# Optimization experiments

Measured on AMD Instinct MI355X. Metric: run time of the kernel, lower is better.

## Reference

```python
import jax, jax.numpy as jnp
from jax import lax
import numpy as np

FDIM = 32          # feature channels
FSIZE = 128        # 2**base_lod, grid has FSIZE+1 points per axis
G = FSIZE + 1
HID = 128          # decoder hidden dim
DOMAIN = 1.2       # FeatureVolume.domain_range
N_PTS = 1_048_576

# 8 corner offsets in (dz, dy, dx) order
_CORNERS = np.array([[0,0,0],[0,0,1],[0,1,0],[0,1,1],
                     [1,0,0],[1,0,1],[1,1,0],[1,1,1]], dtype=np.int32)


def setup_inputs() -> dict:
    key = jax.random.key(0)
    k1, k2, k3, k4, k5, k6 = jax.random.split(key, 6)
    x = jax.random.uniform(k1, (N_PTS, 3), jnp.float32, -DOMAIN, DOMAIN)
    fm = jax.random.normal(k2, (FDIM, G, G, G), jnp.float32) * 0.01
    din = FDIM + 3  # pos_invariant=False -> concat(x, features)
    W1 = jax.random.normal(k3, (HID, din), jnp.float32) * (1.0 / np.sqrt(din))
    b1 = jnp.zeros((HID,), jnp.float32)
    W2 = jax.random.normal(k4, (1, HID), jnp.float32) * (1.0 / np.sqrt(HID))
    b2 = jnp.zeros((1,), jnp.float32)
    return {"x": x, "fm": fm, "W1": W1, "b1": b1, "W2": W2, "b2": b2}


def _trilinear_sample(fm, coords):
    """Faithful jax port of grid_sample_3d (align_corners=True, border clamp).
    fm: [C, ID, IH, IW], coords: [N, 3] in (x, y, z) normalized to [-1, 1].
    Returns [N, C].
    """
    C, ID, IH, IW = fm.shape
    ix = (coords[:, 0] + 1.0) * 0.5 * (IW - 1)
    iy = (coords[:, 1] + 1.0) * 0.5 * (IH - 1)
    iz = (coords[:, 2] + 1.0) * 0.5 * (ID - 1)
    # floors are computed under no_grad in the original
    ix0 = lax.stop_gradient(jnp.floor(ix))
    iy0 = lax.stop_gradient(jnp.floor(iy))
    iz0 = lax.stop_gradient(jnp.floor(iz))
    fx, fy, fz = ix - ix0, iy - iy0, iz - iz0  # fractional offsets, [N]
    wx = jnp.stack([1.0 - fx, fx])  # [2, N]
    wy = jnp.stack([1.0 - fy, fy])
    wz = jnp.stack([1.0 - fz, fz])
    off = jnp.asarray(_CORNERS)  # [8, 3] (dz, dy, dx)
    # per-corner trilinear weights [8, N] (same products as tnw..bse)
    w = wz[off[:, 0]] * wy[off[:, 1]] * wx[off[:, 2]]
    # clamped integer corner indices [8, N]
    xi = jnp.clip(ix0[None] + off[:, 2, None], 0, IW - 1).astype(jnp.int32)
    yi = jnp.clip(iy0[None] + off[:, 1, None], 0, IH - 1).astype(jnp.int32)
    zi = jnp.clip(iz0[None] + off[:, 0, None], 0, ID - 1).astype(jnp.int32)
    flat = (zi * IH + yi) * IW + xi  # [8, N]
    vals = fm.reshape(C, -1)[:, flat]  # [C, 8, N] gather
    return jnp.einsum('ckn,kn->nc', vals, w)


def reference(x, fm, W1, b1, W2, b2):
    # FeatureVolume: normalize by domain_range then trilinear-sample the grid
    feat = _trilinear_sample(fm, x / DOMAIN)          # [N, FDIM]
    ex = jnp.concatenate([x, feat], axis=-1)          # [N, 3 + FDIM]
    h = jax.nn.relu(ex @ W1.T + b1)                   # [N, HID]
    d = h @ W2.T + b2                                 # [N, 1]
    return d.reshape(1, -1, 1)                        # return_dict['pred']
```

## Files before the change

kernel.cpp:

```cpp
#include <hip/hip_runtime.h>
#include <hip/hip_bf16.h>

#define GQ 129
#define S_TOTAL (129*129*129)
#define FDIM 32
#define HID 128
#define DIN 35
#define ROWP 40

__device__ __forceinline__ float bf_lo(unsigned u) { return __uint_as_float(u << 16); }
__device__ __forceinline__ float bf_hi(unsigned u) { return __uint_as_float(u & 0xffff0000u); }

__global__ __launch_bounds__(256) void transpose_vol(const float* __restrict__ fm,
                                                     unsigned* __restrict__ vol)
{
    int s = blockIdx.x * 256 + threadIdx.x;
    if (s >= S_TOTAL) return;
    unsigned pk[16];
#pragma unroll
    for (int j = 0; j < 16; ++j) {
        float a = fm[(size_t)(2*j)     * S_TOTAL + s];
        float b = fm[(size_t)(2*j + 1) * S_TOTAL + s];
        unsigned ua = __float_as_uint(a); ua = (ua + 0x7fffu + ((ua >> 16) & 1u)) >> 16;
        unsigned ub = __float_as_uint(b); ub = (ub + 0x7fffu + ((ub >> 16) & 1u)) >> 16;
        pk[j] = ua | (ub << 16);
    }
    uint4* o = (uint4*)(vol + (size_t)s * 16);
#pragma unroll
    for (int j = 0; j < 4; ++j)
        o[j] = make_uint4(pk[4*j], pk[4*j+1], pk[4*j+2], pk[4*j+3]);
}

__device__ __forceinline__ float mlp_eval(const float* __restrict__ sW1,
                                          const float* __restrict__ sb1,
                                          const float* __restrict__ sW2,
                                          float sb2v,
                                          float px, float py, float pz,
                                          const float feat[FDIM])
{
    float accum = sb2v;
#pragma unroll 4
    for (int h = 0; h < HID; ++h) {
        const float* wr = sW1 + h * ROWP;
        float a = sb1[h];
        a = fmaf(wr[0], px, a);
        a = fmaf(wr[1], py, a);
        a = fmaf(wr[2], pz, a);
        const float4* wf = (const float4*)(wr + 4);
#pragma unroll
        for (int j = 0; j < 8; ++j) {
            float4 w4 = wf[j];
            a = fmaf(w4.x, feat[4*j+0], a);
            a = fmaf(w4.y, feat[4*j+1], a);
            a = fmaf(w4.z, feat[4*j+2], a);
            a = fmaf(w4.w, feat[4*j+3], a);
        }
        accum = fmaf(sW2[h], fmaxf(a, 0.0f), accum);
    }
    return accum;
}

__device__ __forceinline__ void stage_weights(const float* __restrict__ W1,
                                              const float* __restrict__ b1,
                                              const float* __restrict__ W2,
                                              const float* __restrict__ b2,
                                              float* sW1, float* sb1, float* sW2,
                                              float* sb2v)
{
    int t = threadIdx.x;
    for (int i = t; i < HID * DIN; i += 256) {
        int h = i / DIN, c = i % DIN;
        sW1[h * ROWP + (c < 3 ? c : c + 1)] = W1[i];
    }
    if (t < HID) { sb1[t] = b1[t]; sW2[t] = W2[t]; }
    if (t == 0)  { *sb2v = b2[0]; }
    __syncthreads();
}

__global__ __launch_bounds__(256) void sample_mlp(const float* __restrict__ x,
                                                  const unsigned* __restrict__ vol,
                                                  const float* __restrict__ W1,
                                                  const float* __restrict__ b1,
                                                  const float* __restrict__ W2,
                                                  const float* __restrict__ b2,
                                                  float* __restrict__ out, int npts)
{
    __shared__ float sW1[HID * ROWP];
    __shared__ float sb1[HID];
    __shared__ float sW2[HID];
    __shared__ float sb2v;
    stage_weights(W1, b1, W2, b2, sW1, sb1, sW2, &sb2v);

    int p = blockIdx.x * 256 + threadIdx.x;
    if (p >= npts) return;

    float px = x[3*p + 0], py = x[3*p + 1], pz = x[3*p + 2];
    const float SC = 64.0f / 1.2f;
    float ix = fmaf(px, SC, 64.0f);
    float iy = fmaf(py, SC, 64.0f);
    float iz = fmaf(pz, SC, 64.0f);
    float fx0 = floorf(ix), fy0 = floorf(iy), fz0 = floorf(iz);
    float fx = ix - fx0, fy = iy - fy0, fz = iz - fz0;
    int ix0 = (int)fx0, iy0 = (int)fy0, iz0 = (int)fz0;
    int x0 = min(max(ix0, 0), GQ-1), x1 = min(max(ix0 + 1, 0), GQ-1);
    int y0 = min(max(iy0, 0), GQ-1), y1 = min(max(iy0 + 1, 0), GQ-1);
    int z0 = min(max(iz0, 0), GQ-1), z1 = min(max(iz0 + 1, 0), GQ-1);

    float feat[FDIM];
#pragma unroll
    for (int c = 0; c < FDIM; ++c) feat[c] = 0.0f;

#pragma unroll
    for (int k = 0; k < 8; ++k) {
        int zi = (k & 4) ? z1 : z0;
        int yi = (k & 2) ? y1 : y0;
        int xi = (k & 1) ? x1 : x0;
        float w = ((k & 4) ? fz : 1.0f - fz)
                * ((k & 2) ? fy : 1.0f - fy)
                * ((k & 1) ? fx : 1.0f - fx);
        const uint4* q = (const uint4*)(vol + (size_t)((zi * GQ + yi) * GQ + xi) * 16);
#pragma unroll
        for (int j = 0; j < 4; ++j) {
            uint4 v = q[j];
            feat[8*j + 0] = fmaf(w, bf_lo(v.x), feat[8*j + 0]);
            feat[8*j + 1] = fmaf(w, bf_hi(v.x), feat[8*j + 1]);
            feat[8*j + 2] = fmaf(w, bf_lo(v.y), feat[8*j + 2]);
            feat[8*j + 3] = fmaf(w, bf_hi(v.y), feat[8*j + 3]);
            feat[8*j + 4] = fmaf(w, bf_lo(v.z), feat[8*j + 4]);
            feat[8*j + 5] = fmaf(w, bf_hi(v.z), feat[8*j + 5]);
            feat[8*j + 6] = fmaf(w, bf_lo(v.w), feat[8*j + 6]);
            feat[8*j + 7] = fmaf(w, bf_hi(v.w), feat[8*j + 7]);
        }
    }

    out[p] = mlp_eval(sW1, sb1, sW2, sb2v, px, py, pz, feat);
}

__global__ __launch_bounds__(256) void sample_mlp_direct(const float* __restrict__ x,
                                                         const float* __restrict__ fm,
                                                         const float* __restrict__ W1,
                                                         const float* __restrict__ b1,
                                                         const float* __restrict__ W2,
                                                         const float* __restrict__ b2,
                                                         float* __restrict__ out, int npts)
{
    __shared__ float sW1[HID * ROWP];
    __shared__ float sb1[HID];
    __shared__ float sW2[HID];
    __shared__ float sb2v;
    stage_weights(W1, b1, W2, b2, sW1, sb1, sW2, &sb2v);

    int p = blockIdx.x * 256 + threadIdx.x;
    if (p >= npts) return;

    float px = x[3*p + 0], py = x[3*p + 1], pz = x[3*p + 2];
    const float SC = 64.0f / 1.2f;
    float ix = fmaf(px, SC, 64.0f);
    float iy = fmaf(py, SC, 64.0f);
    float iz = fmaf(pz, SC, 64.0f);
    float fx0 = floorf(ix), fy0 = floorf(iy), fz0 = floorf(iz);
    float fx = ix - fx0, fy = iy - fy0, fz = iz - fz0;
    int ix0 = (int)fx0, iy0 = (int)fy0, iz0 = (int)fz0;
    int x0 = min(max(ix0, 0), GQ-1), x1 = min(max(ix0 + 1, 0), GQ-1);
    int y0 = min(max(iy0, 0), GQ-1), y1 = min(max(iy0 + 1, 0), GQ-1);
    int z0 = min(max(iz0, 0), GQ-1), z1 = min(max(iz0 + 1, 0), GQ-1);

    int  sidx[8];
    float cw[8];
#pragma unroll
    for (int k = 0; k < 8; ++k) {
        int zi = (k & 4) ? z1 : z0;
        int yi = (k & 2) ? y1 : y0;
        int xi = (k & 1) ? x1 : x0;
        sidx[k] = (zi * GQ + yi) * GQ + xi;
        cw[k] = ((k & 4) ? fz : 1.0f - fz)
              * ((k & 2) ? fy : 1.0f - fy)
              * ((k & 1) ? fx : 1.0f - fx);
    }

    float feat[FDIM];
#pragma unroll
    for (int c = 0; c < FDIM; ++c) {
        const float* base = fm + (size_t)c * S_TOTAL;
        float a = 0.0f;
#pragma unroll
        for (int k = 0; k < 8; ++k) a = fmaf(cw[k], base[sidx[k]], a);
        feat[c] = a;
    }

    out[p] = mlp_eval(sW1, sb1, sW2, sb2v, px, py, pz, feat);
}

extern "C" void kernel_launch(void* const* d_in, const int* in_sizes, int n_in,
                              void* d_out, int out_size, void* d_ws, size_t ws_size,
                              hipStream_t stream)
{
    const float* x  = (const float*)d_in[0];
    const float* fm = (const float*)d_in[1];
    const float* W1 = (const float*)d_in[2];
    const float* b1 = (const float*)d_in[3];
    const float* W2 = (const float*)d_in[4];
    const float* b2 = (const float*)d_in[5];
    float* out = (float*)d_out;
    int npts = in_sizes[0] / 3;

    size_t need = (size_t)S_TOTAL * FDIM * sizeof(unsigned short);
    if (ws_size >= need) {
        unsigned* vol = (unsigned*)d_ws;
        transpose_vol<<<(S_TOTAL + 255) / 256, 256, 0, stream>>>(fm, vol);
        sample_mlp<<<(npts + 255) / 256, 256, 0, stream>>>(x, vol, W1, b1, W2, b2, out, npts);
    } else {
        sample_mlp_direct<<<(npts + 255) / 256, 256, 0, stream>>>(x, fm, W1, b1, W2, b2, out, npts);
    }
}
```

Measured before the change: 581.8 us.

## Replace scalar MLP with bf16 MFMA over 16-point tiles per wave

Replaces the per-thread scalar FMA decoder with a wave-level bf16 MFMA path. Each wave processes 16 points per tile, with 4 lane groups each gathering an 8-channel slice of the corner features. Positions and their first-layer weights use a hi/lo bf16 split to keep precision. The kernel runs as a grid-stride loop of 512 blocks, keeps the weights in registers instead of LDS, and reduces the second layer with cross-lane shuffles. The trade-off is extra bf16 rounding of the sampled features and an x-load pattern with limited coalescing.

```diff
diff --git a/kernel.cpp b/kernel.cpp
--- a/kernel.cpp
+++ b/kernel.cpp
@@ -8,8 +8,18 @@
 #define DIN 35
 #define ROWP 40
 
+typedef short short8 __attribute__((ext_vector_type(8)));
+typedef float f32x4  __attribute__((ext_vector_type(4)));
+
 __device__ __forceinline__ float bf_lo(unsigned u) { return __uint_as_float(u << 16); }
 __device__ __forceinline__ float bf_hi(unsigned u) { return __uint_as_float(u & 0xffff0000u); }
+__device__ __forceinline__ unsigned short f2bf(float f) {
+    unsigned u = __float_as_uint(f);
+    return (unsigned short)((u + 0x7fffu + ((u >> 16) & 1u)) >> 16);
+}
+__device__ __forceinline__ float bf2f(unsigned short h) {
+    return __uint_as_float(((unsigned)h) << 16);
+}
 
 __global__ __launch_bounds__(256) void transpose_vol(const float* __restrict__ fm,
                                                      unsigned* __restrict__ vol)
@@ -29,6 +39,147 @@
 #pragma unroll
     for (int j = 0; j < 4; ++j)
         o[j] = make_uint4(pk[4*j], pk[4*j+1], pk[4*j+2], pk[4*j+3]);
+}
+
+__global__ __launch_bounds__(256) void sample_mlp_mfma(const float* __restrict__ x,
+                                                       const unsigned* __restrict__ vol,
+                                                       const float* __restrict__ W1,
+                                                       const float* __restrict__ b1,
+                                                       const float* __restrict__ W2,
+                                                       const float* __restrict__ b2,
+                                                       float* __restrict__ out, int npts)
+{
+    const int lane = threadIdx.x & 63;
+    const int wave = blockIdx.x * 4 + (threadIdx.x >> 6);
+    const int nwaves = gridDim.x * 4;
+    const int c = lane & 15;
+    const int g = lane >> 4;
+
+    short8 B0[8], B1[8];
+    float b1v[8], w2v[8];
+#pragma unroll
+    for (int t = 0; t < 8; ++t) {
+        const float* wr = W1 + (t*16 + c) * DIN;
+        short8 f0 = (short8)0, f1 = (short8)0;
+        if (g == 0) {
+            short h0 = (short)f2bf(wr[0]), h1 = (short)f2bf(wr[1]), h2 = (short)f2bf(wr[2]);
+            f0[0] = h0; f0[1] = h1; f0[2] = h2; f0[3] = h0; f0[4] = h1; f0[5] = h2;
+#pragma unroll
+            for (int j = 0; j < 8; ++j) f1[j] = (short)f2bf(wr[3 + 16 + j]);
+        } else if (g == 1) {
+#pragma unroll
+            for (int d = 0; d < 3; ++d) {
+                unsigned short hh = f2bf(wr[d]);
+                f0[d] = (short)f2bf(wr[d] - bf2f(hh));
+            }
+#pragma unroll
+            for (int j = 0; j < 8; ++j) f1[j] = (short)f2bf(wr[3 + 24 + j]);
+        } else if (g == 2) {
+#pragma unroll
+            for (int j = 0; j < 8; ++j) f0[j] = (short)f2bf(wr[3 + j]);
+        } else {
+#pragma unroll
+            for (int j = 0; j < 8; ++j) f0[j] = (short)f2bf(wr[3 + 8 + j]);
+        }
+        B0[t] = f0; B1[t] = f1;
+        b1v[t] = b1[t*16 + c];
+        w2v[t] = W2[t*16 + c];
+    }
+    const float b2v = b2[0];
+
+    const int cb = ((g + 2) & 3) * 8;
+    const char* volb = (const char*)vol + cb * 2;
+
+    const int ntiles = (npts + 15) >> 4;
+    for (int tile = wave; tile < ntiles; tile += nwaves) {
+        const int p0 = tile << 4;
+        const int p  = p0 + c;
+        const int pc = min(p, npts - 1);
+        float px = x[3*pc], py = x[3*pc + 1], pz = x[3*pc + 2];
+        const float SC = 64.0f / 1.2f;
+        float ix = fmaf(px, SC, 64.0f), iy = fmaf(py, SC, 64.0f), iz = fmaf(pz, SC, 64.0f);
+        float fx0 = floorf(ix), fy0 = floorf(iy), fz0 = floorf(iz);
+        float fx = ix - fx0, fy = iy - fy0, fz = iz - fz0;
+        int ix0 = (int)fx0, iy0 = (int)fy0, iz0 = (int)fz0;
+        int x0 = min(max(ix0, 0), GQ-1), x1 = min(max(ix0 + 1, 0), GQ-1);
+        int y0 = min(max(iy0, 0), GQ-1), y1 = min(max(iy0 + 1, 0), GQ-1);
+        int z0 = min(max(iz0, 0), GQ-1), z1 = min(max(iz0 + 1, 0), GQ-1);
+
+        uint4 cv[8]; float w8[8];
+#pragma unroll
+        for (int k = 0; k < 8; ++k) {
+            int zi = (k & 4) ? z1 : z0;
+            int yi = (k & 2) ? y1 : y0;
+            int xi = (k & 1) ? x1 : x0;
+            w8[k] = ((k & 4) ? fz : 1.0f - fz)
+                  * ((k & 2) ? fy : 1.0f - fy)
+                  * ((k & 1) ? fx : 1.0f - fx);
+            cv[k] = *(const uint4*)(volb + (size_t)((zi*GQ + yi)*GQ + xi) * 64);
+        }
+        float F[8];
+#pragma unroll
+        for (int j = 0; j < 8; ++j) F[j] = 0.0f;
+#pragma unroll
+        for (int k = 0; k < 8; ++k) {
+            float w = w8[k]; uint4 v = cv[k];
+            F[0] = fmaf(w, bf_lo(v.x), F[0]); F[1] = fmaf(w, bf_hi(v.x), F[1]);
+            F[2] = fmaf(w, bf_lo(v.y), F[2]); F[3] = fmaf(w, bf_hi(v.y), F[3]);
+            F[4] = fmaf(w, bf_lo(v.z), F[4]); F[5] = fmaf(w, bf_hi(v.z), F[5]);
+            F[6] = fmaf(w, bf_lo(v.w), F[6]); F[7] = fmaf(w, bf_hi(v.w), F[7]);
+        }
+        short8 Fp;
+#pragma unroll
+        for (int j = 0; j < 8; ++j) Fp[j] = (short)f2bf(F[j]);
+
+        short8 A0, A1;
+        if (g < 2) {
+            unsigned short xh0 = f2bf(px), xh1 = f2bf(py), xh2 = f2bf(pz);
+            A0 = (short8)0;
+            A0[0] = (short)xh0; A0[1] = (short)xh1; A0[2] = (short)xh2;
+            if (g == 0) {
+                A0[3] = (short)f2bf(px - bf2f(xh0));
+                A0[4] = (short)f2bf(py - bf2f(xh1));
+                A0[5] = (short)f2bf(pz - bf2f(xh2));
+            }
+            A1 = Fp;
+        } else {
+            A0 = Fp;
+            A1 = (short8)0;
+        }
+
+        f32x4 acc[8];
+#pragma unroll
+        for (int t = 0; t < 8; ++t) { f32x4 z = {0.f, 0.f, 0.f, 0.f}; acc[t] = z; }
+#pragma unroll
+        for (int t = 0; t < 8; ++t) {
+            acc[t] = __builtin_amdgcn_mfma_f32_16x16x32_bf16(A0, B0[t], acc[t], 0, 0, 0);
+            acc[t] = __builtin_amdgcn_mfma_f32_16x16x32_bf16(A1, B1[t], acc[t], 0, 0, 0);
+        }
+
+        float s0 = 0.f, s1 = 0.f, s2 = 0.f, s3 = 0.f;
+#pragma unroll
+        for (int t = 0; t < 8; ++t) {
+            float w2 = w2v[t], bb = b1v[t];
+            s0 = fmaf(w2, fmaxf(acc[t][0] + bb, 0.0f), s0);
+            s1 = fmaf(w2, fmaxf(acc[t][1] + bb, 0.0f), s1);
+            s2 = fmaf(w2, fmaxf(acc[t][2] + bb, 0.0f), s2);
+            s3 = fmaf(w2, fmaxf(acc[t][3] + bb, 0.0f), s3);
+        }
+#pragma unroll
+        for (int m = 1; m < 16; m <<= 1) {
+            s0 += __shfl_xor(s0, m, 64);
+            s1 += __shfl_xor(s1, m, 64);
+            s2 += __shfl_xor(s2, m, 64);
+            s3 += __shfl_xor(s3, m, 64);
+        }
+        if (c < 4) {
+            int pw = p0 + g*4 + c;
+            if (pw < npts) {
+                float sv = (c == 0) ? s0 : (c == 1) ? s1 : (c == 2) ? s2 : s3;
+                out[pw] = sv + b2v;
+            }
+        }
+    }
 }
 
 __device__ __forceinline__ float mlp_eval(const float* __restrict__ sW1,
@@ -69,21 +220,21 @@
 {
     int t = threadIdx.x;
     for (int i = t; i < HID * DIN; i += 256) {
-        int h = i / DIN, c = i % DIN;
-        sW1[h * ROWP + (c < 3 ? c : c + 1)] = W1[i];
+        int h = i / DIN, cc = i % DIN;
+        sW1[h * ROWP + (cc < 3 ? cc : cc + 1)] = W1[i];
     }
     if (t < HID) { sb1[t] = b1[t]; sW2[t] = W2[t]; }
     if (t == 0)  { *sb2v = b2[0]; }
     __syncthreads();
 }
 
-__global__ __launch_bounds__(256) void sample_mlp(const float* __restrict__ x,
-                                                  const unsigned* __restrict__ vol,
-                                                  const float* __restrict__ W1,
-                                                  const float* __restrict__ b1,
-                                                  const float* __restrict__ W2,
-                                                  const float* __restrict__ b2,
-                                                  float* __restrict__ out, int npts)
+__global__ __launch_bounds__(256) void sample_mlp_direct(const float* __restrict__ x,
+                                                         const float* __restrict__ fm,
+                                                         const float* __restrict__ W1,
+                                                         const float* __restrict__ b1,
+                                                         const float* __restrict__ W2,
+                                                         const float* __restrict__ b2,
+                                                         float* __restrict__ out, int npts)
 {
     __shared__ float sW1[HID * ROWP];
     __shared__ float sb1[HID];
@@ -106,65 +257,6 @@
     int y0 = min(max(iy0, 0), GQ-1), y1 = min(max(iy0 + 1, 0), GQ-1);
     int z0 = min(max(iz0, 0), GQ-1), z1 = min(max(iz0 + 1, 0), GQ-1);
 
-    float feat[FDIM];
-#pragma unroll
-    for (int c = 0; c < FDIM; ++c) feat[c] = 0.0f;
-
-#pragma unroll
-    for (int k = 0; k < 8; ++k) {
-        int zi = (k & 4) ? z1 : z0;
-        int yi = (k & 2) ? y1 : y0;
-        int xi = (k & 1) ? x1 : x0;
-        float w = ((k & 4) ? fz : 1.0f - fz)
-                * ((k & 2) ? fy : 1.0f - fy)
-                * ((k & 1) ? fx : 1.0f - fx);
-        const uint4* q = (const uint4*)(vol + (size_t)((zi * GQ + yi) * GQ + xi) * 16);
-#pragma unroll
-        for (int j = 0; j < 4; ++j) {
-            uint4 v = q[j];
-            feat[8*j + 0] = fmaf(w, bf_lo(v.x), feat[8*j + 0]);
-            feat[8*j + 1] = fmaf(w, bf_hi(v.x), feat[8*j + 1]);
-            feat[8*j + 2] = fmaf(w, bf_lo(v.y), feat[8*j + 2]);
-            feat[8*j + 3] = fmaf(w, bf_hi(v.y), feat[8*j + 3]);
-            feat[8*j + 4] = fmaf(w, bf_lo(v.z), feat[8*j + 4]);
-            feat[8*j + 5] = fmaf(w, bf_hi(v.z), feat[8*j + 5]);
-            feat[8*j + 6] = fmaf(w, bf_lo(v.w), feat[8*j + 6]);
-            feat[8*j + 7] = fmaf(w, bf_hi(v.w), feat[8*j + 7]);
-        }
-    }
-
-    out[p] = mlp_eval(sW1, sb1, sW2, sb2v, px, py, pz, feat);
-}
-
-__global__ __launch_bounds__(256) void sample_mlp_direct(const float* __restrict__ x,
-                                                         const float* __restrict__ fm,
-                                                         const float* __restrict__ W1,
-                                                         const float* __restrict__ b1,
-                                                         const float* __restrict__ W2,
-                                                         const float* __restrict__ b2,
-                                                         float* __restrict__ out, int npts)
-{
-    __shared__ float sW1[HID * ROWP];
-    __shared__ float sb1[HID];
-    __shared__ float sW2[HID];
-    __shared__ float sb2v;
-    stage_weights(W1, b1, W2, b2, sW1, sb1, sW2, &sb2v);
-
-    int p = blockIdx.x * 256 + threadIdx.x;
-    if (p >= npts) return;
-
-    float px = x[3*p + 0], py = x[3*p + 1], pz = x[3*p + 2];
-    const float SC = 64.0f / 1.2f;
-    float ix = fmaf(px, SC, 64.0f);
-    float iy = fmaf(py, SC, 64.0f);
-    float iz = fmaf(pz, SC, 64.0f);
-    float fx0 = floorf(ix), fy0 = floorf(iy), fz0 = floorf(iz);
-    float fx = ix - fx0, fy = iy - fy0, fz = iz - fz0;
-    int ix0 = (int)fx0, iy0 = (int)fy0, iz0 = (int)fz0;
-    int x0 = min(max(ix0, 0), GQ-1), x1 = min(max(ix0 + 1, 0), GQ-1);
-    int y0 = min(max(iy0, 0), GQ-1), y1 = min(max(iy0 + 1, 0), GQ-1);
-    int z0 = min(max(iz0, 0), GQ-1), z1 = min(max(iz0 + 1, 0), GQ-1);
-
     int  sidx[8];
     float cw[8];
 #pragma unroll
@@ -180,12 +272,12 @@
 
     float feat[FDIM];
 #pragma unroll
-    for (int c = 0; c < FDIM; ++c) {
-        const float* base = fm + (size_t)c * S_TOTAL;
+    for (int cc = 0; cc < FDIM; ++cc) {
+        const float* base = fm + (size_t)cc * S_TOTAL;
         float a = 0.0f;
 #pragma unroll
         for (int k = 0; k < 8; ++k) a = fmaf(cw[k], base[sidx[k]], a);
-        feat[c] = a;
+        feat[cc] = a;
     }
 
     out[p] = mlp_eval(sW1, sb1, sW2, sb2v, px, py, pz, feat);
@@ -208,7 +300,7 @@
     if (ws_size >= need) {
         unsigned* vol = (unsigned*)d_ws;
         transpose_vol<<<(S_TOTAL + 255) / 256, 256, 0, stream>>>(fm, vol);
-        sample_mlp<<<(npts + 255) / 256, 256, 0, stream>>>(x, vol, W1, b1, W2, b2, out, npts);
+        sample_mlp_mfma<<<512, 256, 0, stream>>>(x, vol, W1, b1, W2, b2, out, npts);
     } else {
         sample_mlp_direct<<<(npts + 255) / 256, 256, 0, stream>>>(x, fm, W1, b1, W2, b2, out, npts);
     }
```

New measurement: 523.6 us. 10.0% less time.
